# Optimization experiments

Measured on AMD Instinct MI355X. Metric: run time of the kernel, lower is better.

The kernel has to match this reference:

```python
import jax, jax.numpy as jnp
import numpy as np

B, TOPK, E, C, K = 64, 2, 16, 1024, 4096


def setup_inputs() -> dict:
    key = jax.random.key(0)
    k1, k2, k3, k4, k5, k6 = jax.random.split(key, 6)
    return {
        "activated": jax.random.normal(k1, (B, TOPK, K), dtype=jnp.float32),
        "expert_indices": jax.random.randint(k2, (B, TOPK), 0, E, dtype=jnp.int64)
        if jax.config.jax_enable_x64 else jax.random.randint(k2, (B, TOPK), 0, E, dtype=jnp.int32),
        "expert_weights": jax.random.uniform(k3, (B, TOPK), dtype=jnp.float32),
        "mlp2_weight": jax.random.normal(k4, (E, C, K), dtype=jnp.float32),
        "mlp2_bias": jax.random.normal(k5, (E, C), dtype=jnp.float32),
        "residual_x": jax.random.normal(k6, (B, C), dtype=jnp.float32),
    }


def reference(activated, expert_indices, expert_weights, mlp2_weight, mlp2_bias, residual_x):
    # Gather per-token expert weights/biases: w [B, topk, C, K], b [B, topk, C]
    w = mlp2_weight[expert_indices]
    b = mlp2_bias[expert_indices]
    # Batched matvec per (token, expert slot): t [B, topk, C]
    t = jnp.einsum("beck,bek->bec", w, activated) + b
    # Weighted combine over top-k expert slots, plus residual: [B, C]
    return residual_x + jnp.einsum("bec,be->bc", t, expert_weights)
```

## Files before the change

### kernel.cpp

```cpp
#include <hip/hip_runtime.h>

#define BB    64
#define TOPK  2
#define EE    16
#define CC    1024
#define KK    4096

constexpr int RPB = 16;
constexpr int P   = 16;
constexpr int KS  = 2;
constexpr int KH  = KK / KS;
constexpr int NW  = KH / 4 / 64;

typedef float v4f __attribute__((ext_vector_type(4)));

__global__ __launch_bounds__(256) void route_init(
    const int* __restrict__ idx, const float* __restrict__ ew,
    const float* __restrict__ bias, const float* __restrict__ resid,
    float* __restrict__ out, int* __restrict__ cnt, int* __restrict__ lists)
{
    if (blockIdx.x == 0) {
        __shared__ int scnt[EE];
        if (threadIdx.x < EE) scnt[threadIdx.x] = 0;
        __syncthreads();
        if (threadIdx.x < BB * TOPK) {
            int e = idx[threadIdx.x];
            int pos = atomicAdd(&scnt[e], 1);
            lists[e * 128 + pos] = threadIdx.x;
        }
        __syncthreads();
        if (threadIdx.x < EE) cnt[threadIdx.x] = scnt[threadIdx.x];
    } else {
        int i = (blockIdx.x - 1) * 256 + threadIdx.x;
        int b = i >> 10;
        int c = i & (CC - 1);
        float v = resid[i];
#pragma unroll
        for (int s = 0; s < TOPK; s++) {
            int e = idx[b * TOPK + s];
            v += ew[b * TOPK + s] * bias[e * CC + c];
        }
        out[i] = v;
    }
}

__global__ __launch_bounds__(256) void moe_mlp2(
    const float* __restrict__ act, const float* __restrict__ ew,
    const float* __restrict__ W, float* __restrict__ out,
    const int* __restrict__ cnt, const int* __restrict__ lists)
{
    const int bid = blockIdx.x;
    const int e = bid >> 7;
    const int n = cnt[e];
    if (n == 0) return;
    const int ct = (bid >> 1) & 63;
    const int ks = bid & 1;
    const int c0   = ct * RPB;
    const int lane = threadIdx.x & 63;
    const int wave = threadIdx.x >> 6;
    const int row0 = c0 + wave * 4;
    const v4f* __restrict__ Wb =
        (const v4f*)(W + (size_t)(e * CC + row0) * KK + ks * KH);
    const char* __restrict__ actb = (const char*)(act + ks * KH);

    for (int g = 0; g < n; g += P) {
        const int np = min(P, n - g);

        int aoff[P];
        int pid[P];
#pragma unroll
        for (int p = 0; p < P; p++) {
            pid[p]  = (p < np) ? lists[e * 128 + g + p] : 0;
            aoff[p] = pid[p] * (KK * 4);
        }

        float acc[4][P];
#pragma unroll
        for (int r = 0; r < 4; r++)
#pragma unroll
            for (int p = 0; p < P; p++) acc[r][p] = 0.f;

#pragma unroll 2
        for (int kw = 0; kw < NW; kw++) {
            const int fi = kw * 64 + lane;
            v4f w4[4];
#pragma unroll
            for (int r = 0; r < 4; r++)
                w4[r] = __builtin_nontemporal_load(Wb + (size_t)r * (KK / 4) + fi);
            const char* abase = actb + ((size_t)fi << 4);
#pragma unroll
            for (int pc = 0; pc < P / 4; pc++) {
                if (pc * 4 < np) {
#pragma unroll
                    for (int j = 0; j < 4; j++) {
                        const int p = pc * 4 + j;
                        const v4f a = *(const v4f*)(abase + aoff[p]);
#pragma unroll
                        for (int r = 0; r < 4; r++)
                            acc[r][p] += w4[r].x * a.x + w4[r].y * a.y +
                                         w4[r].z * a.z + w4[r].w * a.w;
                    }
                }
            }
        }

#pragma unroll
        for (int p = 0; p < P; p++) {
            if (p < np) {
                float v0 = acc[0][p], v1 = acc[1][p];
                float v2 = acc[2][p], v3 = acc[3][p];
#pragma unroll
                for (int off = 32; off > 0; off >>= 1) {
                    v0 += __shfl_down(v0, off, 64);
                    v1 += __shfl_down(v1, off, 64);
                    v2 += __shfl_down(v2, off, 64);
                    v3 += __shfl_down(v3, off, 64);
                }
                if (lane == 0) {
                    int pr = pid[p];
                    float w = ew[pr];
                    float* o = out + (pr >> 1) * CC + row0;
                    atomicAdd(o + 0, w * v0);
                    atomicAdd(o + 1, w * v1);
                    atomicAdd(o + 2, w * v2);
                    atomicAdd(o + 3, w * v3);
                }
            }
        }
    }
}

extern "C" void kernel_launch(void* const* d_in, const int* in_sizes, int n_in,
                              void* d_out, int out_size, void* d_ws, size_t ws_size,
                              hipStream_t stream) {
    const float* act   = (const float*)d_in[0];
    const int*   idx   = (const int*)d_in[1];
    const float* ew    = (const float*)d_in[2];
    const float* W     = (const float*)d_in[3];
    const float* bias  = (const float*)d_in[4];
    const float* resid = (const float*)d_in[5];
    float* out = (float*)d_out;

    int* cnt   = (int*)d_ws;
    int* lists = (int*)d_ws + 64;

    route_init<<<1 + (BB * CC) / 256, 256, 0, stream>>>(
        idx, ew, bias, resid, out, cnt, lists);
    moe_mlp2<<<EE * (CC / RPB) * KS, 256, 0, stream>>>(
        act, ew, W, out, cnt, lists);
}
```

Baseline: 397.4 us.

## Preload expert weights into registers and stage activations in LDS

Doubles the K split to four so each block handles a smaller K slice, then issues all of a wave's weight loads up front into registers instead of streaming them inside the loop. Token activations for each group are copied into a 64KB shared-memory tile with direct global-to-LDS loads, replacing repeated scattered global reads. The aim is more outstanding memory requests and better bandwidth on the weight stream. The cost is higher register and LDS use per block, which lowers occupancy, plus twice as many atomic partial-sum adds to the output.

```diff
diff --git a/kernel.cpp b/kernel.cpp
--- a/kernel.cpp
+++ b/kernel.cpp
@@ -8,7 +8,7 @@
 
 constexpr int RPB = 16;
 constexpr int P   = 16;
-constexpr int KS  = 2;
+constexpr int KS  = 4;
 constexpr int KH  = KK / KS;
 constexpr int NW  = KH / 4 / 64;
 
@@ -49,30 +49,42 @@
     const float* __restrict__ W, float* __restrict__ out,
     const int* __restrict__ cnt, const int* __restrict__ lists)
 {
+    __shared__ float sact[P][KH];
+
     const int bid = blockIdx.x;
-    const int e = bid >> 7;
-    const int n = cnt[e];
+    const int e   = bid >> 8;
+    const int n   = cnt[e];
     if (n == 0) return;
-    const int ct = (bid >> 1) & 63;
-    const int ks = bid & 1;
-    const int c0   = ct * RPB;
+    const int ct   = (bid >> 2) & 63;
+    const int ks   = bid & 3;
     const int lane = threadIdx.x & 63;
     const int wave = threadIdx.x >> 6;
-    const int row0 = c0 + wave * 4;
+    const int row0 = ct * RPB + wave * 4;
+
     const v4f* __restrict__ Wb =
         (const v4f*)(W + (size_t)(e * CC + row0) * KK + ks * KH);
-    const char* __restrict__ actb = (const char*)(act + ks * KH);
+    v4f w[4][NW];
+#pragma unroll
+    for (int r = 0; r < 4; r++)
+#pragma unroll
+        for (int kw = 0; kw < NW; kw++)
+            w[r][kw] = __builtin_nontemporal_load(
+                Wb + (size_t)r * (KK / 4) + kw * 64 + lane);
 
     for (int g = 0; g < n; g += P) {
         const int np = min(P, n - g);
+        if (g) __syncthreads();
 
-        int aoff[P];
-        int pid[P];
-#pragma unroll
-        for (int p = 0; p < P; p++) {
-            pid[p]  = (p < np) ? lists[e * 128 + g + p] : 0;
-            aoff[p] = pid[p] * (KK * 4);
+        for (int p = 0; p < np; p++) {
+            int pr = lists[e * 128 + g + p];
+            const float* gsrc =
+                act + (size_t)pr * KK + ks * KH + (wave * 64 + lane) * 4;
+            __builtin_amdgcn_global_load_lds(
+                (const __attribute__((address_space(1))) void*)gsrc,
+                (__attribute__((address_space(3))) void*)&sact[p][wave * 256],
+                16, 0, 0);
         }
+        __syncthreads();
 
         float acc[4][P];
 #pragma unroll
@@ -80,25 +92,20 @@
 #pragma unroll
             for (int p = 0; p < P; p++) acc[r][p] = 0.f;
 
-#pragma unroll 2
+#pragma unroll
         for (int kw = 0; kw < NW; kw++) {
-            const int fi = kw * 64 + lane;
-            v4f w4[4];
-#pragma unroll
-            for (int r = 0; r < 4; r++)
-                w4[r] = __builtin_nontemporal_load(Wb + (size_t)r * (KK / 4) + fi);
-            const char* abase = actb + ((size_t)fi << 4);
+            const int fb = (kw * 64 + lane) * 4;
 #pragma unroll
             for (int pc = 0; pc < P / 4; pc++) {
                 if (pc * 4 < np) {
 #pragma unroll
                     for (int j = 0; j < 4; j++) {
                         const int p = pc * 4 + j;
-                        const v4f a = *(const v4f*)(abase + aoff[p]);
+                        const v4f a = *(const v4f*)&sact[p][fb];
 #pragma unroll
                         for (int r = 0; r < 4; r++)
-                            acc[r][p] += w4[r].x * a.x + w4[r].y * a.y +
-                                         w4[r].z * a.z + w4[r].w * a.w;
+                            acc[r][p] += w[r][kw].x * a.x + w[r][kw].y * a.y +
+                                         w[r][kw].z * a.z + w[r][kw].w * a.w;
                     }
                 }
             }
@@ -117,13 +124,13 @@
                     v3 += __shfl_down(v3, off, 64);
                 }
                 if (lane == 0) {
-                    int pr = pid[p];
-                    float w = ew[pr];
+                    int pr = lists[e * 128 + g + p];
+                    float wgt = ew[pr];
                     float* o = out + (pr >> 1) * CC + row0;
-                    atomicAdd(o + 0, w * v0);
-                    atomicAdd(o + 1, w * v1);
-                    atomicAdd(o + 2, w * v2);
-                    atomicAdd(o + 3, w * v3);
+                    atomicAdd(o + 0, wgt * v0);
+                    atomicAdd(o + 1, wgt * v1);
+                    atomicAdd(o + 2, wgt * v2);
+                    atomicAdd(o + 3, wgt * v3);
                 }
             }
         }
```

After: 394.9 us. No clear change (-0.6%).
